# Kernel optimization log

Hardware: AMD Instinct MI355X
Metric: run time of the kernel (lower is better)

## Reference

```python
import jax, jax.numpy as jnp
import numpy as np

B, T, D = 2, 2048, 1024
H, W = 16, 256  # n_head, window_size
HD = D // H


def setup_inputs() -> dict:
    key = jax.random.key(0)
    ks = jax.random.split(key, 5)
    s = 0.02
    return {
        "x": jax.random.normal(ks[0], (B, T, D), dtype=jnp.float32),
        "Wqkv": jax.random.normal(ks[1], (3 * D, D), dtype=jnp.float32) * s,
        "bqkv": jax.random.normal(ks[2], (3 * D,), dtype=jnp.float32) * s,
        "Wo": jax.random.normal(ks[3], (D, D), dtype=jnp.float32) * s,
        "bo": jax.random.normal(ks[4], (D,), dtype=jnp.float32) * s,
    }


def reference(x, Wqkv, bqkv, Wo, bo):
    b, t, d = x.shape
    qkv = x @ Wqkv.T + bqkv  # [b, t, 3d]
    # rearrange 'b t (c h d) -> c b h t d'
    qkv = qkv.reshape(b, t, 3, H, HD)
    q = jnp.transpose(qkv[:, :, 0], (0, 2, 1, 3))  # [b, h, t, hd]
    k = jnp.transpose(qkv[:, :, 1], (0, 2, 1, 3))
    v = jnp.transpose(qkv[:, :, 2], (0, 2, 1, 3))
    scores = jnp.einsum('bhid,bhjd->bhij', q, k) / jnp.sqrt(jnp.float32(HD))
    i = jnp.arange(t)[:, None]
    j = jnp.arange(t)[None, :]
    # tril(diag=0) & triu(diag=-(W-1)): j <= i and j >= i - (W-1)
    mask = (j <= i) & (j >= i - (W - 1))
    scores = jnp.where(mask, scores, -jnp.inf)
    probs = jax.nn.softmax(scores, axis=-1)
    y = jnp.einsum('bhij,bhjd->bhid', probs, v)
    y = jnp.transpose(y, (0, 2, 1, 3)).reshape(b, t, d)  # b h t d -> b t (h d)
    return y @ Wo.T + bo
```

## Files before the change

kernel.cpp:

```cpp
#include <hip/hip_runtime.h>
#include <hip/hip_bf16.h>
#include <stdint.h>


typedef __attribute__((ext_vector_type(8))) short short8;
typedef __attribute__((ext_vector_type(4))) float f32x4;

#define MFMA16(a, b, c) __builtin_amdgcn_mfma_f32_16x16x32_bf16((a), (b), (c), 0, 0, 0)

static __device__ __forceinline__ void gl_lds16(const void* g, void* l) {
  __builtin_amdgcn_global_load_lds(
      (const __attribute__((address_space(1))) unsigned int*)g,
      (__attribute__((address_space(3))) unsigned int*)l, 16, 0, 0);
}

#define LGKM0 do { asm volatile("s_waitcnt lgkmcnt(0)" ::: "memory"); \
                   __builtin_amdgcn_sched_barrier(0); } while (0)
#define BARM do { asm volatile("" ::: "memory"); \
                  __builtin_amdgcn_s_barrier(); \
                  asm volatile("" ::: "memory"); } while (0)

static __device__ __forceinline__ uint32_t pkbf(float x, float y) {
  union { __hip_bfloat16 h; uint16_t u; } a, b;
  a.h = __float2bfloat16(x);
  b.h = __float2bfloat16(y);
  return (uint32_t)a.u | ((uint32_t)b.u << 16);
}

__global__ void cvt_all(const float* __restrict__ x, const float* __restrict__ wqkv,
                        const float* __restrict__ wo, __hip_bfloat16* __restrict__ xb,
                        __hip_bfloat16* __restrict__ wqkvb,
                        __hip_bfloat16* __restrict__ wob) {
  const int N0 = 524288, N1 = 393216, N2 = 131072;
  int i = blockIdx.x * blockDim.x + threadIdx.x;
  const int stride = gridDim.x * blockDim.x;
  for (; i < N0 + N1 + N2; i += stride) {
    const float* in;
    __hip_bfloat16* out;
    int gidx;
    if (i < N0) { in = x; out = xb; gidx = i; }
    else if (i < N0 + N1) { in = wqkv; out = wqkvb; gidx = i - N0; }
    else { in = wo; out = wob; gidx = i - N0 - N1; }
    const float4* p = (const float4*)in + (size_t)gidx * 2;
    float4 v0 = p[0], v1 = p[1];
    union { short8 s; __hip_bfloat16 h[8]; } u;
    u.h[0] = __float2bfloat16(v0.x); u.h[1] = __float2bfloat16(v0.y);
    u.h[2] = __float2bfloat16(v0.z); u.h[3] = __float2bfloat16(v0.w);
    u.h[4] = __float2bfloat16(v1.x); u.h[5] = __float2bfloat16(v1.y);
    u.h[6] = __float2bfloat16(v1.z); u.h[7] = __float2bfloat16(v1.w);
    ((short8*)out)[gidx] = u.s;
  }
}

__global__ __launch_bounds__(512, 4) void gemm_qkv(
    const __hip_bfloat16* __restrict__ A, const __hip_bfloat16* __restrict__ Bm,
    const float* __restrict__ bias,
    __hip_bfloat16* __restrict__ qb, __hip_bfloat16* __restrict__ kb,
    __hip_bfloat16* __restrict__ vt2) {
  __shared__ alignas(128) char smem[81920];
  const int tid = threadIdx.x;
  const int lane = tid & 63, w = tid >> 6;
  const int wm = w >> 2, wn = w & 3;
  const int r = lane & 15, g = lane >> 4;
  const int K = 1024, NT = 16;

  const int cpx = gridDim.x >> 3;
  const int swzb = (blockIdx.x & 7) * cpx + (blockIdx.x >> 3);
  const int bm = swzb >> 4, bn = swzb & 15;

  const int srow = tid >> 3;
  const int e = (tid & 7) ^ ((tid >> 4) & 7);
  const int koff = (e >> 2) * 32 + (e & 3) * 8;
  const __hip_bfloat16* aU[2];
  const __hip_bfloat16* bU[3];
#pragma unroll
  for (int U = 0; U < 2; ++U)
    aU[U] = A + (size_t)(bm * 128 + U * 64 + srow) * K + koff;
#pragma unroll
  for (int U = 0; U < 3; ++U)
    bU[U] = Bm + (size_t)(bn * 192 + U * 64 + srow) * K + koff;
  const int ldst = tid * 16;

#define STA(t, U) gl_lds16(aU[U] + (t) * 64, smem + ((t) & 1) * 40960 + (U) * 8192 + ldst)
#define STB(t, U) gl_lds16(bU[U] + (t) * 64, smem + ((t) & 1) * 40960 + 16384 + (U) * 8192 + ldst)

  const int hsw = (r >> 1) & 7;
  const int s0 = ((0 + g) ^ hsw) * 16;
  const int s1 = ((4 + g) ^ hsw) * 16;
  const int rdA = (wm * 64 + r) * 128;
  const int rdB = 16384 + (wn * 48 + r) * 128;

  f32x4 acc[4][3] = {};
  short8 af[4][2], bf[3][2];

  STA(0, 0); STA(0, 1); STB(0, 0); STB(0, 1); STB(0, 2);
  STA(1, 0); STA(1, 1); STB(1, 0); STB(1, 1); STB(1, 2);
  asm volatile("s_waitcnt vmcnt(5)" ::: "memory");
  BARM;

#pragma unroll 1
  for (int t = 0; t < NT; ++t) {
    const char* cb = smem + (t & 1) * 40960;
#pragma unroll
    for (int i = 0; i < 4; ++i) {
      af[i][0] = *(const short8*)(cb + rdA + i * 2048 + s0);
      af[i][1] = *(const short8*)(cb + rdA + i * 2048 + s1);
    }
#pragma unroll
    for (int j = 0; j < 3; ++j) {
      bf[j][0] = *(const short8*)(cb + rdB + j * 2048 + s0);
      bf[j][1] = *(const short8*)(cb + rdB + j * 2048 + s1);
    }
    LGKM0;
    __builtin_amdgcn_s_setprio(1);
#pragma unroll
    for (int i = 0; i < 4; ++i)
#pragma unroll
      for (int j = 0; j < 3; ++j) acc[i][j] = MFMA16(af[i][0], bf[j][0], acc[i][j]);
#pragma unroll
    for (int i = 0; i < 4; ++i)
#pragma unroll
      for (int j = 0; j < 3; ++j) acc[i][j] = MFMA16(af[i][1], bf[j][1], acc[i][j]);
    __builtin_amdgcn_s_setprio(0);
    BARM;
    if (t + 2 < NT) {
      STB(t + 2, 0); STB(t + 2, 1); STB(t + 2, 2);
      STA(t + 2, 0); STA(t + 2, 1);
      asm volatile("s_waitcnt vmcnt(5)" ::: "memory");
    } else if (t + 1 < NT) {
      asm volatile("s_waitcnt vmcnt(0)" ::: "memory");
    }
    BARM;
  }
#undef STA
#undef STB

  float bjv[3];
  const int nb = bn * 192 + wn * 48;
#pragma unroll
  for (int j = 0; j < 3; ++j) bjv[j] = bias[nb + j * 16 + r];
#pragma unroll
  for (int i = 0; i < 4; ++i) {
    const int m0 = bm * 128 + wm * 64 + i * 16 + g * 4;
#pragma unroll
    for (int j = 0; j < 3; ++j) {
      const int nn = nb + j * 16 + r;
      const int c = nn >> 10, h = (nn >> 6) & 15, hd = nn & 63;
      const int b_ = m0 >> 11, t0 = m0 & 2047;
      const size_t hb = (size_t)(b_ * 16 + h);
      if (c == 0) {
#pragma unroll
        for (int q = 0; q < 4; ++q)
          qb[(hb * 2048 + t0 + q) * 64 + hd] =
              __float2bfloat16((acc[i][j][q] + bjv[j]) * 0.125f);
      } else if (c == 1) {
#pragma unroll
        for (int q = 0; q < 4; ++q)
          kb[(hb * 2048 + t0 + q) * 64 + hd] =
              __float2bfloat16(acc[i][j][q] + bjv[j]);
      } else {
        union { uint2 u; __hip_bfloat16 hh[4]; } pk;
#pragma unroll
        for (int q = 0; q < 4; ++q)
          pk.hh[q] = __float2bfloat16(acc[i][j][q] + bjv[j]);
        const int kk = t0 & 31;
        const int pp = ((kk & 12) << 1) + ((kk & 16) >> 2);
        *(uint2*)&vt2[hb * 131072 + (size_t)(t0 >> 5) * 2048 + hd * 32 + pp] =
            pk.u;
      }
    }
  }
}

__global__ __launch_bounds__(512, 4) void gemm_out8(
    const __hip_bfloat16* __restrict__ A, const __hip_bfloat16* __restrict__ Bm,
    const float* __restrict__ bias, float* __restrict__ outF) {
  __shared__ alignas(128) char smem[65536];
  const int tid = threadIdx.x;
  const int lane = tid & 63, w = tid >> 6;
  const int wm = w >> 2, wn = w & 3;
  const int r = lane & 15, g = lane >> 4;
  const int K = 1024, NT = 16;

  const int cpx = gridDim.x >> 3;
  const int swzb = (blockIdx.x & 7) * cpx + (blockIdx.x >> 3);
  const int bm = swzb >> 3, bn = swzb & 7;

  const int srow = tid >> 3;
  const int e = (tid & 7) ^ ((tid >> 4) & 7);
  const int koff = (e >> 2) * 32 + (e & 3) * 8;
  const __hip_bfloat16* aU[2];
  const __hip_bfloat16* bU[2];
#pragma unroll
  for (int U = 0; U < 2; ++U) {
    aU[U] = A + (size_t)(bm * 128 + U * 64 + srow) * K + koff;
    bU[U] = Bm + (size_t)(bn * 128 + U * 64 + srow) * K + koff;
  }
  const int ldst = tid * 16;

#define STA(t, U) gl_lds16(aU[U] + (t) * 64, smem + ((t) & 1) * 32768 + (U) * 8192 + ldst)
#define STB(t, U) gl_lds16(bU[U] + (t) * 64, smem + ((t) & 1) * 32768 + 16384 + (U) * 8192 + ldst)

  const int hsw = (r >> 1) & 7;
  const int s0 = ((0 + g) ^ hsw) * 16;
  const int s1 = ((4 + g) ^ hsw) * 16;
  const int rdA = (wm * 64 + r) * 128;
  const int rdB = 16384 + (wn * 32 + r) * 128;

  f32x4 acc[4][2] = {};
  short8 af[4][2], bf[2][2];

  STA(0, 0); STA(0, 1); STB(0, 0); STB(0, 1);
  STA(1, 0); STA(1, 1); STB(1, 0); STB(1, 1);
  asm volatile("s_waitcnt vmcnt(4)" ::: "memory");
  BARM;

#pragma unroll 1
  for (int t = 0; t < NT; ++t) {
    const char* cb = smem + (t & 1) * 32768;
#pragma unroll
    for (int i = 0; i < 4; ++i) {
      af[i][0] = *(const short8*)(cb + rdA + i * 2048 + s0);
      af[i][1] = *(const short8*)(cb + rdA + i * 2048 + s1);
    }
#pragma unroll
    for (int j = 0; j < 2; ++j) {
      bf[j][0] = *(const short8*)(cb + rdB + j * 2048 + s0);
      bf[j][1] = *(const short8*)(cb + rdB + j * 2048 + s1);
    }
    LGKM0;
    __builtin_amdgcn_s_setprio(1);
#pragma unroll
    for (int i = 0; i < 4; ++i)
#pragma unroll
      for (int j = 0; j < 2; ++j) acc[i][j] = MFMA16(af[i][0], bf[j][0], acc[i][j]);
#pragma unroll
    for (int i = 0; i < 4; ++i)
#pragma unroll
      for (int j = 0; j < 2; ++j) acc[i][j] = MFMA16(af[i][1], bf[j][1], acc[i][j]);
    __builtin_amdgcn_s_setprio(0);
    BARM;
    if (t + 2 < NT) {
      STB(t + 2, 0); STB(t + 2, 1);
      STA(t + 2, 0); STA(t + 2, 1);
      asm volatile("s_waitcnt vmcnt(4)" ::: "memory");
    } else if (t + 1 < NT) {
      asm volatile("s_waitcnt vmcnt(0)" ::: "memory");
    }
    BARM;
  }
#undef STA
#undef STB

  float bjv[2];
  const int nb = bn * 128 + wn * 32;
#pragma unroll
  for (int j = 0; j < 2; ++j) bjv[j] = bias[nb + j * 16 + r];
#pragma unroll
  for (int i = 0; i < 4; ++i) {
    const int m0 = bm * 128 + wm * 64 + i * 16 + g * 4;
#pragma unroll
    for (int j = 0; j < 2; ++j) {
      const int nn = nb + j * 16 + r;
#pragma unroll
      for (int q = 0; q < 4; ++q)
        outF[(size_t)(m0 + q) * 1024 + nn] = acc[i][j][q] + bjv[j];
    }
  }
}

__global__ __launch_bounds__(512, 6) void attn_local(
    const __hip_bfloat16* __restrict__ qb, const __hip_bfloat16* __restrict__ kb,
    const __hip_bfloat16* __restrict__ vt2, __hip_bfloat16* __restrict__ yb) {
  __shared__ alignas(16) char smem[49152];
  const int xcd = blockIdx.x & 7;
  const int idx = blockIdx.x >> 3;
  const int bh = xcd + (idx >> 4) * 8;
  const int qt = idx & 15;
  const int tid = threadIdx.x;
  const int w = tid >> 6, lane = tid & 63;
  const int r = lane & 15, g = lane >> 4;
  const int qa = qt * 128 + w * 16;

  const __hip_bfloat16* qp = qb + (size_t)bh * 2048 * 64;
  const __hip_bfloat16* kp = kb + (size_t)bh * 2048 * 64;
  const __hip_bfloat16* vpb = vt2 + (size_t)bh * 131072 + r * 32 + g * 8;

  const int t_lo = (qt >= 2) ? (4 * qt - 8) : 0;
  const int t_hi = 4 * qt + 3;
  const int nunits = (t_hi - t_lo + 1) << 8;
#pragma unroll
  for (int rr = 0; rr < 6; ++rr) {
    const int u = rr * 512 + tid;
    if (u < nunits) {
      const int tt = u >> 8, row = (u >> 3) & 31, sl = u & 7;
      gl_lds16(kp + (size_t)((t_lo + tt) * 32 + row) * 64 + (sl ^ (row & 7)) * 8,
               smem + u * 16);
    }
  }

  const short8 qf0 = *(const short8*)&qp[(qa + r) * 64 + g * 8];
  const short8 qf1 = *(const short8*)&qp[(qa + r) * 64 + g * 8 + 32];

  asm volatile("s_waitcnt vmcnt(0)" ::: "memory");
  __syncthreads();

  f32x4 acc[4] = {};
  float m = -1e30f;
  float lsum = 0.f;

  const int wlo = ((qa >= 256) ? ((qa - 255) >> 5) : 0) - t_lo;
  const int whi = ((qa + 15) >> 5) - t_lo;
  const int xsw = (r & 7) << 4;

#pragma unroll 1
  for (int tt = wlo; tt <= whi; ++tt) {
    const int tabs = t_lo + tt;
    const int kbase = tabs << 5;
    const short8 v0 = *(const short8*)(vpb + (size_t)tabs * 2048);
    const short8 v1 = *(const short8*)(vpb + (size_t)tabs * 2048 + 512);
    const short8 v2 = *(const short8*)(vpb + (size_t)tabs * 2048 + 1024);
    const short8 v3 = *(const short8*)(vpb + (size_t)tabs * 2048 + 1536);
    const char* kt = smem + tt * 4096;
    const short8 k00 = *(const short8*)(kt + r * 128 + (((g) << 4) ^ xsw));
    const short8 k01 = *(const short8*)(kt + r * 128 + (((4 + g) << 4) ^ xsw));
    const short8 k10 = *(const short8*)(kt + (16 + r) * 128 + (((g) << 4) ^ xsw));
    const short8 k11 = *(const short8*)(kt + (16 + r) * 128 + (((4 + g) << 4) ^ xsw));
    f32x4 st0 = {}, st1 = {};
    __builtin_amdgcn_s_setprio(1);
    st0 = MFMA16(k00, qf0, st0);
    st0 = MFMA16(k01, qf1, st0);
    st1 = MFMA16(k10, qf0, st1);
    st1 = MFMA16(k11, qf1, st1);
    __builtin_amdgcn_s_setprio(0);
    float sv[2][4];
#pragma unroll
    for (int q = 0; q < 4; ++q) {
      const unsigned d0 = (unsigned)(qa + r) - (unsigned)(kbase + g * 4 + q);
      const unsigned d1 = (unsigned)(qa + r) - (unsigned)(kbase + 16 + g * 4 + q);
      sv[0][q] = (d0 <= 255u) ? st0[q] : -1e30f;
      sv[1][q] = (d1 <= 255u) ? st1[q] : -1e30f;
    }
    const float tmax = fmaxf(
        fmaxf(fmaxf(sv[0][0], sv[0][1]), fmaxf(sv[0][2], sv[0][3])),
        fmaxf(fmaxf(sv[1][0], sv[1][1]), fmaxf(sv[1][2], sv[1][3])));
    if (!__all(tmax <= m + 8.f)) {
      float rm = tmax;
      rm = fmaxf(rm, __shfl_xor(rm, 16));
      rm = fmaxf(rm, __shfl_xor(rm, 32));
      const float mnew = fmaxf(m, rm);
      const float fac = __expf(m - mnew);
      m = mnew;
      lsum *= fac;
      acc[0] *= fac; acc[1] *= fac; acc[2] *= fac; acc[3] *= fac;
    }
    float p[2][4];
#pragma unroll
    for (int f = 0; f < 2; ++f)
#pragma unroll
      for (int q = 0; q < 4; ++q) {
        p[f][q] = __expf(sv[f][q] - m);
        lsum += p[f][q];
      }
    union { short8 s; uint32_t u[4]; } pb;
    pb.u[0] = pkbf(p[0][0], p[0][1]);
    pb.u[1] = pkbf(p[0][2], p[0][3]);
    pb.u[2] = pkbf(p[1][0], p[1][1]);
    pb.u[3] = pkbf(p[1][2], p[1][3]);
    __builtin_amdgcn_s_setprio(1);
    acc[0] = MFMA16(v0, pb.s, acc[0]);
    acc[1] = MFMA16(v1, pb.s, acc[1]);
    acc[2] = MFMA16(v2, pb.s, acc[2]);
    acc[3] = MFMA16(v3, pb.s, acc[3]);
    __builtin_amdgcn_s_setprio(0);
  }

  lsum += __shfl_xor(lsum, 16);
  lsum += __shfl_xor(lsum, 32);
  const float inv = 1.f / lsum;

  const int b_ = bh >> 4, h = bh & 15;
  __hip_bfloat16* yrow = yb + (size_t)(b_ * 2048 + qa + r) * 1024 + h * 64;
#pragma unroll
  for (int u = 0; u < 4; ++u) {
    union { uint2 uu; __hip_bfloat16 hh[4]; } pk;
#pragma unroll
    for (int q = 0; q < 4; ++q) pk.hh[q] = __float2bfloat16(acc[u][q] * inv);
    *(uint2*)&yrow[u * 16 + g * 4] = pk.uu;
  }
}

extern "C" void kernel_launch(void* const* d_in, const int* in_sizes, int n_in,
                              void* d_out, int out_size, void* d_ws,
                              size_t ws_size, hipStream_t stream) {
  const float* x = (const float*)d_in[0];
  const float* Wqkv = (const float*)d_in[1];
  const float* bqkv = (const float*)d_in[2];
  const float* Wo = (const float*)d_in[3];
  const float* bo = (const float*)d_in[4];
  float* out = (float*)d_out;

  char* ws = (char*)d_ws;
  __hip_bfloat16* xb = (__hip_bfloat16*)(ws + 0);
  __hip_bfloat16* wqkvb = (__hip_bfloat16*)(ws + 8388608);
  __hip_bfloat16* wob = (__hip_bfloat16*)(ws + 14680064);
  __hip_bfloat16* qb = (__hip_bfloat16*)(ws + 16777216);
  __hip_bfloat16* kb = (__hip_bfloat16*)(ws + 25165824);
  __hip_bfloat16* vt2 = (__hip_bfloat16*)(ws + 33554432);
  __hip_bfloat16* yb = (__hip_bfloat16*)(ws + 41943040);

  cvt_all<<<2048, 256, 0, stream>>>(x, Wqkv, Wo, xb, wqkvb, wob);

  gemm_qkv<<<512, 512, 0, stream>>>(xb, wqkvb, bqkv, qb, kb, vt2);
  attn_local<<<512, 512, 0, stream>>>(qb, kb, vt2, yb);
  gemm_out8<<<256, 512, 0, stream>>>(yb, wob, bo, out);
}
```

Measured before the change: 72.47 us.

## Fuse fp32-to-bf16 conversion into GEMM tile staging, drop cvt_all kernel

```diff
diff --git a/kernel.cpp b/kernel.cpp
--- a/kernel.cpp
+++ b/kernel.cpp
@@ -27,33 +27,17 @@
   return (uint32_t)a.u | ((uint32_t)b.u << 16);
 }
 
-__global__ void cvt_all(const float* __restrict__ x, const float* __restrict__ wqkv,
-                        const float* __restrict__ wo, __hip_bfloat16* __restrict__ xb,
-                        __hip_bfloat16* __restrict__ wqkvb,
-                        __hip_bfloat16* __restrict__ wob) {
-  const int N0 = 524288, N1 = 393216, N2 = 131072;
-  int i = blockIdx.x * blockDim.x + threadIdx.x;
-  const int stride = gridDim.x * blockDim.x;
-  for (; i < N0 + N1 + N2; i += stride) {
-    const float* in;
-    __hip_bfloat16* out;
-    int gidx;
-    if (i < N0) { in = x; out = xb; gidx = i; }
-    else if (i < N0 + N1) { in = wqkv; out = wqkvb; gidx = i - N0; }
-    else { in = wo; out = wob; gidx = i - N0 - N1; }
-    const float4* p = (const float4*)in + (size_t)gidx * 2;
-    float4 v0 = p[0], v1 = p[1];
-    union { short8 s; __hip_bfloat16 h[8]; } u;
-    u.h[0] = __float2bfloat16(v0.x); u.h[1] = __float2bfloat16(v0.y);
-    u.h[2] = __float2bfloat16(v0.z); u.h[3] = __float2bfloat16(v0.w);
-    u.h[4] = __float2bfloat16(v1.x); u.h[5] = __float2bfloat16(v1.y);
-    u.h[6] = __float2bfloat16(v1.z); u.h[7] = __float2bfloat16(v1.w);
-    ((short8*)out)[gidx] = u.s;
-  }
+static __device__ __forceinline__ short8 cvt8(float4 lo, float4 hi) {
+  union { short8 s; __hip_bfloat16 h[8]; } u;
+  u.h[0] = __float2bfloat16(lo.x); u.h[1] = __float2bfloat16(lo.y);
+  u.h[2] = __float2bfloat16(lo.z); u.h[3] = __float2bfloat16(lo.w);
+  u.h[4] = __float2bfloat16(hi.x); u.h[5] = __float2bfloat16(hi.y);
+  u.h[6] = __float2bfloat16(hi.z); u.h[7] = __float2bfloat16(hi.w);
+  return u.s;
 }
 
 __global__ __launch_bounds__(512, 4) void gemm_qkv(
-    const __hip_bfloat16* __restrict__ A, const __hip_bfloat16* __restrict__ Bm,
+    const float* __restrict__ X, const float* __restrict__ WQKV,
     const float* __restrict__ bias,
     __hip_bfloat16* __restrict__ qb, __hip_bfloat16* __restrict__ kb,
     __hip_bfloat16* __restrict__ vt2) {
@@ -62,7 +46,7 @@
   const int lane = tid & 63, w = tid >> 6;
   const int wm = w >> 2, wn = w & 3;
   const int r = lane & 15, g = lane >> 4;
-  const int K = 1024, NT = 16;
+  const int NT = 16;
 
   const int cpx = gridDim.x >> 3;
   const int swzb = (blockIdx.x & 7) * cpx + (blockIdx.x >> 3);
@@ -71,18 +55,36 @@
   const int srow = tid >> 3;
   const int e = (tid & 7) ^ ((tid >> 4) & 7);
   const int koff = (e >> 2) * 32 + (e & 3) * 8;
-  const __hip_bfloat16* aU[2];
-  const __hip_bfloat16* bU[3];
+  const float* aF[2];
+  const float* bF[3];
 #pragma unroll
   for (int U = 0; U < 2; ++U)
-    aU[U] = A + (size_t)(bm * 128 + U * 64 + srow) * K + koff;
+    aF[U] = X + (size_t)(bm * 128 + U * 64 + srow) * 1024 + koff;
 #pragma unroll
   for (int U = 0; U < 3; ++U)
-    bU[U] = Bm + (size_t)(bn * 192 + U * 64 + srow) * K + koff;
+    bF[U] = WQKV + (size_t)(bn * 192 + U * 64 + srow) * 1024 + koff;
   const int ldst = tid * 16;
 
-#define STA(t, U) gl_lds16(aU[U] + (t) * 64, smem + ((t) & 1) * 40960 + (U) * 8192 + ldst)
-#define STB(t, U) gl_lds16(bU[U] + (t) * 64, smem + ((t) & 1) * 40960 + 16384 + (U) * 8192 + ldst)
+  auto STAGE = [&](int tt) {
+    char* db = smem + ((tt) & 1) * 40960;
+    float4 tA[2][2], tB[3][2];
+#pragma unroll
+    for (int U = 0; U < 2; ++U) {
+      tA[U][0] = *(const float4*)(aF[U] + tt * 64);
+      tA[U][1] = *(const float4*)(aF[U] + tt * 64 + 4);
+    }
+#pragma unroll
+    for (int U = 0; U < 3; ++U) {
+      tB[U][0] = *(const float4*)(bF[U] + tt * 64);
+      tB[U][1] = *(const float4*)(bF[U] + tt * 64 + 4);
+    }
+#pragma unroll
+    for (int U = 0; U < 2; ++U)
+      *(short8*)(db + U * 8192 + ldst) = cvt8(tA[U][0], tA[U][1]);
+#pragma unroll
+    for (int U = 0; U < 3; ++U)
+      *(short8*)(db + 16384 + U * 8192 + ldst) = cvt8(tB[U][0], tB[U][1]);
+  };
 
   const int hsw = (r >> 1) & 7;
   const int s0 = ((0 + g) ^ hsw) * 16;
@@ -93,9 +95,9 @@
   f32x4 acc[4][3] = {};
   short8 af[4][2], bf[3][2];
 
-  STA(0, 0); STA(0, 1); STB(0, 0); STB(0, 1); STB(0, 2);
-  STA(1, 0); STA(1, 1); STB(1, 0); STB(1, 1); STB(1, 2);
-  asm volatile("s_waitcnt vmcnt(5)" ::: "memory");
+  STAGE(0);
+  STAGE(1);
+  LGKM0;
   BARM;
 
 #pragma unroll 1
@@ -124,16 +126,11 @@
     __builtin_amdgcn_s_setprio(0);
     BARM;
     if (t + 2 < NT) {
-      STB(t + 2, 0); STB(t + 2, 1); STB(t + 2, 2);
-      STA(t + 2, 0); STA(t + 2, 1);
-      asm volatile("s_waitcnt vmcnt(5)" ::: "memory");
-    } else if (t + 1 < NT) {
-      asm volatile("s_waitcnt vmcnt(0)" ::: "memory");
+      STAGE(t + 2);
+      LGKM0;
     }
     BARM;
   }
-#undef STA
-#undef STB
 
   float bjv[3];
   const int nb = bn * 192 + wn * 48;
@@ -173,7 +170,7 @@
 }
 
 __global__ __launch_bounds__(512, 4) void gemm_out8(
-    const __hip_bfloat16* __restrict__ A, const __hip_bfloat16* __restrict__ Bm,
+    const __hip_bfloat16* __restrict__ A, const float* __restrict__ WO,
     const float* __restrict__ bias, float* __restrict__ outF) {
   __shared__ alignas(128) char smem[65536];
   const int tid = threadIdx.x;
@@ -190,16 +187,28 @@
   const int e = (tid & 7) ^ ((tid >> 4) & 7);
   const int koff = (e >> 2) * 32 + (e & 3) * 8;
   const __hip_bfloat16* aU[2];
-  const __hip_bfloat16* bU[2];
+  const float* bFo[2];
 #pragma unroll
   for (int U = 0; U < 2; ++U) {
     aU[U] = A + (size_t)(bm * 128 + U * 64 + srow) * K + koff;
-    bU[U] = Bm + (size_t)(bn * 128 + U * 64 + srow) * K + koff;
+    bFo[U] = WO + (size_t)(bn * 128 + U * 64 + srow) * 1024 + koff;
   }
   const int ldst = tid * 16;
 
-#define STA(t, U) gl_lds16(aU[U] + (t) * 64, smem + ((t) & 1) * 32768 + (U) * 8192 + ldst)
-#define STB(t, U) gl_lds16(bU[U] + (t) * 64, smem + ((t) & 1) * 32768 + 16384 + (U) * 8192 + ldst)
+  auto STG = [&](int tt) {
+    char* db = smem + ((tt) & 1) * 32768;
+    float4 tB[2][2];
+#pragma unroll
+    for (int U = 0; U < 2; ++U) {
+      tB[U][0] = *(const float4*)(bFo[U] + tt * 64);
+      tB[U][1] = *(const float4*)(bFo[U] + tt * 64 + 4);
+    }
+    gl_lds16(aU[0] + tt * 64, db + 0 * 8192 + ldst);
+    gl_lds16(aU[1] + tt * 64, db + 1 * 8192 + ldst);
+#pragma unroll
+    for (int U = 0; U < 2; ++U)
+      *(short8*)(db + 16384 + U * 8192 + ldst) = cvt8(tB[U][0], tB[U][1]);
+  };
 
   const int hsw = (r >> 1) & 7;
   const int s0 = ((0 + g) ^ hsw) * 16;
@@ -210,9 +219,10 @@
   f32x4 acc[4][2] = {};
   short8 af[4][2], bf[2][2];
 
-  STA(0, 0); STA(0, 1); STB(0, 0); STB(0, 1);
-  STA(1, 0); STA(1, 1); STB(1, 0); STB(1, 1);
-  asm volatile("s_waitcnt vmcnt(4)" ::: "memory");
+  STG(0);
+  STG(1);
+  asm volatile("s_waitcnt vmcnt(0)" ::: "memory");
+  LGKM0;
   BARM;
 
 #pragma unroll 1
@@ -241,16 +251,13 @@
     __builtin_amdgcn_s_setprio(0);
     BARM;
     if (t + 2 < NT) {
-      STB(t + 2, 0); STB(t + 2, 1);
-      STA(t + 2, 0); STA(t + 2, 1);
-      asm volatile("s_waitcnt vmcnt(4)" ::: "memory");
+      STG(t + 2);
+      LGKM0;
     } else if (t + 1 < NT) {
       asm volatile("s_waitcnt vmcnt(0)" ::: "memory");
     }
     BARM;
   }
-#undef STA
-#undef STB
 
   float bjv[2];
   const int nb = bn * 128 + wn * 32;
@@ -401,17 +408,12 @@
   float* out = (float*)d_out;
 
   char* ws = (char*)d_ws;
-  __hip_bfloat16* xb = (__hip_bfloat16*)(ws + 0);
-  __hip_bfloat16* wqkvb = (__hip_bfloat16*)(ws + 8388608);
-  __hip_bfloat16* wob = (__hip_bfloat16*)(ws + 14680064);
-  __hip_bfloat16* qb = (__hip_bfloat16*)(ws + 16777216);
-  __hip_bfloat16* kb = (__hip_bfloat16*)(ws + 25165824);
-  __hip_bfloat16* vt2 = (__hip_bfloat16*)(ws + 33554432);
-  __hip_bfloat16* yb = (__hip_bfloat16*)(ws + 41943040);
-
-  cvt_all<<<2048, 256, 0, stream>>>(x, Wqkv, Wo, xb, wqkvb, wob);
-
-  gemm_qkv<<<512, 512, 0, stream>>>(xb, wqkvb, bqkv, qb, kb, vt2);
+  __hip_bfloat16* qb = (__hip_bfloat16*)(ws + 0);
+  __hip_bfloat16* kb = (__hip_bfloat16*)(ws + 8388608);
+  __hip_bfloat16* vt2 = (__hip_bfloat16*)(ws + 16777216);
+  __hip_bfloat16* yb = (__hip_bfloat16*)(ws + 25165824);
+
+  gemm_qkv<<<512, 512, 0, stream>>>(x, Wqkv, bqkv, qb, kb, vt2);
   attn_local<<<512, 512, 0, stream>>>(qb, kb, vt2, yb);
-  gemm_out8<<<256, 512, 0, stream>>>(yb, wob, bo, out);
-}
+  gemm_out8<<<256, 512, 0, stream>>>(yb, Wo, bo, out);
+}
```

Result: slower. 84.59 us (+16.7%).
